# Performance work log

Hardware: AMD Instinct MI355X
Metric: run time of the kernel (lower is better)

## Reference

```python
import jax, jax.numpy as jnp
import numpy as np

D, H, K, L, NB = 128, 8, 16, 16, 2
N, E, MN, ME = 100_000, 800_000, 1_000, 8_000
VOCAB, BT, VP = 50_000, 256, 15
_SQD, _SQK = float(np.sqrt(D)), float(np.sqrt(K))


def _segment_softmax(score, seg, num):
    m = jax.ops.segment_max(score, seg, num_segments=num)
    e = jnp.exp(score - m[seg])
    z = jax.ops.segment_sum(e, seg, num_segments=num)
    return e / (z[seg] + 1e-9)


def _meta_learner(feat, u, W2, W1):
    # latent-attention factorization: feat [n,D] -> 2d param [n,H,K], 1d param [n,H]
    w = jax.nn.softmax((feat @ u.T) / _SQD, axis=-1)  # [n,L]
    return jnp.einsum('nl,lhk->nhk', w, W2), w @ W1


def _conv(feat, src, dst, p2n, p1n, p2e, p1e, Wq, Wk, Wv, Wo):
    # HeteroAttnConv: multi-head attention message passing modulated by
    # per-node (p2n,p1n) and per-edge (p2e,p1e) meta parameters.
    n = feat.shape[0]
    q = (feat @ Wq).reshape(n, H, K) * p2n
    kf = (feat @ Wk).reshape(n, H, K)
    v = (feat @ Wv).reshape(n, H, K)
    ke = kf[src] * p2e                                   # [e,H,K]
    score = (q[dst] * ke).sum(-1) / _SQK + p1e + p1n[dst]  # [e,H]
    attn = _segment_softmax(score, dst, n)
    agg = jax.ops.segment_sum(attn[..., None] * v[src], dst, num_segments=n).reshape(n, D)
    return jax.nn.relu(agg @ Wo), ke.reshape(-1, D)


def _forward(emb, u, W2lat, W1lat, Wq_m, Wk_m, Wv_m, Wo_m, Wq, Wk, Wv, Wo,
             node_vals, meta_node_vals, src, dst, meta_src, meta_dst,
             meta_node_id, meta_edge_id, target_idx,
             static_vals, static_src, static_dst):
    # _init_meta_param: static param-name graph, copy_u/sum then meta_learner
    fs = emb[static_vals]
    agg = jax.ops.segment_sum(fs[static_src], static_dst, num_segments=VP)
    p2s, p1s = _meta_learner(agg, u, W2lat, W1lat)
    base_tw, base_n1, base_n2 = p1s[0], p1s[3], p2s[6]   # target_weight, node 1d, node 2d
    base_e1, base_e2 = p1s[9], p2s[12]                   # edge 1d, edge 2d

    meta_feat = emb[meta_node_vals]
    feat = emb[node_vals]
    # _asign_param_to_graph(meta_graph): broadcast base buffers only
    mp2n = jnp.broadcast_to(base_n2, (MN, H, K))
    mp1n = jnp.broadcast_to(base_n1, (MN, H))
    mp2e = jnp.broadcast_to(base_e2, (ME, H, K))
    mp1e = jnp.broadcast_to(base_e1, (ME, H))

    out = jnp.zeros((BT, 1), feat.dtype)
    for b in range(NB):
        pre_meta, pre = meta_feat, feat
        meta_feat, meta_edge_feat = _conv(meta_feat, meta_src, meta_dst,
                                          mp2n, mp1n, mp2e, mp1e,
                                          Wq_m[b], Wk_m[b], Wv_m[b], Wo_m[b])
        # _asign_param_to_graph(graph, meta_node_feat, meta_edge_feat):
        # base repeat + indexed add of meta_learner outputs
        p2mn, p1mn = _meta_learner(meta_feat, u, W2lat, W1lat)
        p2me, p1me = _meta_learner(meta_edge_feat, u, W2lat, W1lat)
        p2n = base_n2[None] + p2mn[meta_node_id]
        p1n = base_n1[None] + p1mn[meta_node_id]
        tw = base_tw[None] + p1mn[meta_node_id]
        p2e = base_e2[None] + p2me[meta_edge_id]
        p1e = base_e1[None] + p1me[meta_edge_id]
        feat, _ = _conv(feat, src, dst, p2n, p1n, p2e, p1e,
                        Wq[b], Wk[b], Wv[b], Wo[b])
        # block residual
        meta_feat = meta_feat + pre_meta
        feat = feat + pre
        # Target: per-target-node weighted readout with target_weight param
        logit = jnp.einsum('th,thk->t', tw[target_idx],
                           feat[target_idx].reshape(BT, H, K))
        out = out + logit[:, None]
    return out / NB


def setup_inputs() -> dict:
    key = jax.random.key(0)
    ks = jax.random.split(key, 24)
    s = 0.05
    inp = {}
    inp['emb'] = jax.random.normal(ks[0], (VOCAB, D), jnp.float32) * s
    inp['u'] = jax.random.normal(ks[1], (L, D), jnp.float32) * s
    inp['W2lat'] = jax.random.normal(ks[2], (L, H, K), jnp.float32) * s
    inp['W1lat'] = jax.random.normal(ks[3], (L, H), jnp.float32) * s
    for i, nm in enumerate(['Wq_m', 'Wk_m', 'Wv_m', 'Wo_m', 'Wq', 'Wk', 'Wv', 'Wo']):
        inp[nm] = jax.random.normal(ks[4 + i], (NB, D, D), jnp.float32) / np.sqrt(D)
    inp['node_vals'] = jax.random.randint(ks[12], (N,), 0, VOCAB)
    inp['meta_node_vals'] = jax.random.randint(ks[13], (MN,), 0, VOCAB)
    inp['src'] = jax.random.randint(ks[14], (E,), 0, N)
    inp['dst'] = jax.random.randint(ks[15], (E,), 0, N)
    inp['meta_src'] = jax.random.randint(ks[16], (ME,), 0, MN)
    inp['meta_dst'] = jax.random.randint(ks[17], (ME,), 0, MN)
    inp['meta_node_id'] = jax.random.randint(ks[18], (N,), 0, MN)
    inp['meta_edge_id'] = jax.random.randint(ks[19], (E,), 0, ME)
    inp['target_idx'] = jax.random.randint(ks[20], (BT,), 0, N)
    # static param-name graph: 5 names x (1 name node + 2 token nodes), tokens->name
    name_pos = np.arange(5) * 3
    inp['static_vals'] = jax.random.randint(ks[21], (VP,), 0, VOCAB)
    inp['static_src'] = jnp.asarray(np.stack([name_pos + 1, name_pos + 2], 1).reshape(-1), jnp.int32)
    inp['static_dst'] = jnp.asarray(np.repeat(name_pos, 2), jnp.int32)
    return inp


def reference(emb, u, W2lat, W1lat, Wq_m, Wk_m, Wv_m, Wo_m, Wq, Wk, Wv, Wo,
              node_vals, meta_node_vals, src, dst, meta_src, meta_dst,
              meta_node_id, meta_edge_id, target_idx,
              static_vals, static_src, static_dst):
    return _forward(emb, u, W2lat, W1lat, Wq_m, Wk_m, Wv_m, Wo_m, Wq, Wk, Wv, Wo,
                    node_vals, meta_node_vals, src, dst, meta_src, meta_dst,
                    meta_node_id, meta_edge_id, target_idx,
                    static_vals, static_src, static_dst)
```

## Files before the change

### kernel.cpp

```cpp
#include <hip/hip_runtime.h>
#include <hip/hip_bf16.h>
#include <hip/hip_fp8.h>

#define DD   128
#define HH   8

typedef short bf16x8 __attribute__((ext_vector_type(8)));
typedef float f32x4  __attribute__((ext_vector_type(4)));
typedef float f32x2  __attribute__((ext_vector_type(2)));

__device__ __forceinline__ float b2f(unsigned short v){
  union { unsigned int u; float f; } x; x.u = ((unsigned int)v) << 16; return x.f;
}
__device__ __forceinline__ unsigned short f2b(float f){
  __hip_bfloat16 h = __float2bfloat16(f);
  return *(unsigned short*)&h;
}
__device__ __forceinline__ unsigned char f2f8(float x){
  __hip_fp8_e4m3 h(x);
  return h.__x;
}
__device__ __forceinline__ float f82f(unsigned char b){
  __hip_fp8_e4m3 h; h.__x = b;
  return (float)h;
}
__device__ __forceinline__ void cvt4(unsigned int w, float* o){
#if defined(__has_builtin)
# if __has_builtin(__builtin_amdgcn_cvt_pk_f32_fp8)
  f32x2 lo = __builtin_amdgcn_cvt_pk_f32_fp8((int)w, false);
  f32x2 hi = __builtin_amdgcn_cvt_pk_f32_fp8((int)w, true);
  o[0]=lo[0]; o[1]=lo[1]; o[2]=hi[0]; o[3]=hi[1];
  return;
# endif
#endif
  o[0]=f82f(w&0xff); o[1]=f82f((w>>8)&0xff);
  o[2]=f82f((w>>16)&0xff); o[3]=f82f((w>>24)&0xff);
}
struct __align__(8) us4 { unsigned short x,y,z,w; };
struct __align__(16) us8 { unsigned short s[8]; };

__device__ __forceinline__ float gld(const void* p, size_t i, bool f32){
  if (f32) return ((const float*)p)[i];
  return b2f(((const unsigned short*)p)[i]);
}

__device__ __forceinline__ void gll16(const void* g, void* l){
  __builtin_amdgcn_global_load_lds(
      (const __attribute__((address_space(1))) unsigned int*)g,
      (__attribute__((address_space(3))) unsigned int*)l, 16, 0, 0);
}

struct WPtrs { const void* p[8]; };
__global__ __launch_bounds__(256) void w_repack16(
    WPtrs W, unsigned short* __restrict__ stage, int NBt,
    const int* __restrict__ dflag)
{
  const bool wf32 = (*dflag) != 0;
  int idx = blockIdx.x >> 6;
  int ti = idx / NBt, bi = idx - ti*NBt;
  size_t bo = (size_t)bi*DD*DD;
  int i = (blockIdx.x & 63)*256 + threadIdx.x;
  int k = i >> 7, n = i & 127;
  float x;
  if (wf32) x = ((const float*)W.p[ti])[bo + i];
  else      x = b2f(((const unsigned short*)W.p[ti])[bo + i]);
  stage[(size_t)idx*DD*DD + n*DD + k] = f2b(x);
}

enum { EPI_STORE=0, EPI_SCALE_CONST=1, EPI_RELU=3,
       EPI_RELU_RES=4, EPI_RELU_RES2=5 };

#define CPAD 132


template<int EPI, bool INB, bool OUTB>
__global__ __launch_bounds__(256) void gemm128m(
    const void* __restrict__ Av, const unsigned short* __restrict__ Bt,
    void* __restrict__ Cv, int M,
    const unsigned short* __restrict__ Rb,
    const float* __restrict__ Rf, float* __restrict__ C2)
{
  __shared__ __align__(16) unsigned short Asb[64*128];
  __shared__ __align__(16) unsigned short Btb[16896];
  const int tid = threadIdx.x;
  const int wave = tid >> 6, lane = tid & 63;
  const int row0 = blockIdx.x * 64;

  if (INB){
    const char* Ab = (const char*)Av;
    int n4 = lane >> 4, c = lane & 15;
#pragma unroll
    for (int op=0; op<4; op++){
      int rA = wave*16 + op*4;
      int n = rA + n4;
      int gr = row0 + n; if (gr >= M) gr = M - 1;
      gll16(Ab + (size_t)gr*256 + ((size_t)((c ^ (n & 7)) << 4)), &Asb[rA*128]);
    }
  } else {
    const float* Af = (const float*)Av;
    int r = tid >> 2, cb = (tid & 3) * 32, rx = (r & 7) << 3;
    int gr = row0 + r;
#pragma unroll
    for (int j=0;j<8;j++){
      int cc = cb + j*4;
      float4 val = make_float4(0.f,0.f,0.f,0.f);
      if (gr < M) val = *(const float4*)(Af + (size_t)gr*DD + cc);
      us4 o; o.x=f2b(val.x); o.y=f2b(val.y); o.z=f2b(val.z); o.w=f2b(val.w);
      *(us4*)&Asb[r*128 + (cc ^ rx)] = o;
    }
  }
  {
    int n4 = lane >> 4, c = lane & 15;
#pragma unroll
    for (int op=0; op<8; op++){
      int rB = wave*32 + op*4;
      int n = rB + n4;
      gll16((const char*)Bt + (size_t)n*256 + ((size_t)((c ^ (n & 7)) << 4)),
            &Btb[rB*128]);
    }
  }
  __syncthreads();

  f32x4 acc[8];
#pragma unroll
  for (int t=0;t<8;t++) acc[t] = (f32x4){0.f,0.f,0.f,0.f};
  const int am = (lane & 15), kq = (lane >> 4) * 8, axr = (am & 7) << 3;
#pragma unroll
  for (int k0=0;k0<128;k0+=32){
    int xo = (k0 + kq) ^ axr;
    bf16x8 a = *(bf16x8*)&Asb[(wave*16 + am)*128 + xo];
#pragma unroll
    for (int t=0;t<8;t++){
      bf16x8 b = *(bf16x8*)&Btb[(t*16 + am)*128 + xo];
      acc[t] = __builtin_amdgcn_mfma_f32_16x16x32_bf16(a, b, acc[t], 0,0,0);
    }
  }
  __syncthreads();
  float* Cls = (float*)Btb;
  {
    int rr = wave*16 + (lane>>4)*4;
    int cc = lane & 15;
#pragma unroll
    for (int t=0;t<8;t++)
#pragma unroll
      for (int r=0;r<4;r++)
        Cls[(rr + r)*CPAD + t*16 + cc] = acc[t][r];
  }
  __syncthreads();

  {
    int r = tid >> 2, cb = (tid & 3) * 32;
    int gr = row0 + r;
    if (gr < M){
#pragma unroll
      for (int j=0;j<8;j++){
        int c = cb + j*4;
        float4 o = *(float4*)&Cls[r*CPAD + c];
        if (EPI == EPI_RELU_RES){
          us4 rb = *(const us4*)(Rb + (size_t)gr*DD + c);
          o.x=fmaxf(o.x,0.f)+b2f(rb.x); o.y=fmaxf(o.y,0.f)+b2f(rb.y);
          o.z=fmaxf(o.z,0.f)+b2f(rb.z); o.w=fmaxf(o.w,0.f)+b2f(rb.w);
        } else if (EPI == EPI_RELU_RES2){
          o.x=fmaxf(o.x,0.f); o.y=fmaxf(o.y,0.f); o.z=fmaxf(o.z,0.f); o.w=fmaxf(o.w,0.f);
          float4 rf = *(const float4*)(Rf + (size_t)gr*DD + c);
          *(float4*)(C2 + (size_t)gr*DD + c) =
              make_float4(o.x+rf.x, o.y+rf.y, o.z+rf.z, o.w+rf.w);
        }
        if (OUTB){
          us4 ob; ob.x=f2b(o.x); ob.y=f2b(o.y); ob.z=f2b(o.z); ob.w=f2b(o.w);
          *(us4*)((unsigned short*)Cv + (size_t)gr*DD + c) = ob;
        } else {
          *(float4*)((float*)Cv + (size_t)gr*DD + c) = o;
        }
      }
    }
  }
}

template<int EPIQ, bool INB, bool FP8KV>
__device__ __forceinline__ void qkv_body(
    unsigned short* Asb, unsigned short* Btb, int blk,
    const void* __restrict__ Av,
    const unsigned short* __restrict__ Btq, const unsigned short* __restrict__ Btk,
    const unsigned short* __restrict__ Btv,
    void* __restrict__ Cq, void* __restrict__ Ck, int stK,
    void* __restrict__ Cvo, int stV, int M,
    const float* __restrict__ svec)
{
  const int tid = threadIdx.x;
  const int wave = tid >> 6, lane = tid & 63;
  const int row0 = blk * 64;

  if (INB){
    const char* Ab = (const char*)Av;
    int n4 = lane >> 4, c = lane & 15;
#pragma unroll
    for (int op=0; op<4; op++){
      int rA = wave*16 + op*4;
      int n = rA + n4;
      int gr = row0 + n; if (gr >= M) gr = M - 1;
      gll16(Ab + (size_t)gr*256 + ((size_t)((c ^ (n & 7)) << 4)), &Asb[rA*128]);
    }
  } else {
    const float* Af = (const float*)Av;
    int r = tid >> 2, cb = (tid & 3) * 32, rx = (r & 7) << 3;
    int gr = row0 + r;
#pragma unroll
    for (int j=0;j<8;j++){
      int cc = cb + j*4;
      float4 val = make_float4(0.f,0.f,0.f,0.f);
      if (gr < M) val = *(const float4*)(Af + (size_t)gr*DD + cc);
      us4 o; o.x=f2b(val.x); o.y=f2b(val.y); o.z=f2b(val.z); o.w=f2b(val.w);
      *(us4*)&Asb[r*128 + (cc ^ rx)] = o;
    }
  }

  const unsigned short* Bts[3] = {Btq, Btk, Btv};
  void* Cs[3] = {Cq, Ck, Cvo};
  const int sts[3] = {DD, stK, stV};
  const int am = (lane & 15), kq = (lane >> 4) * 8, axr = (am & 7) << 3;

  for (int ph=0; ph<3; ph++){
    {
      const unsigned short* Bt = Bts[ph];
      int n4 = lane >> 4, c = lane & 15;
#pragma unroll
      for (int op=0; op<8; op++){
        int rB = wave*32 + op*4;
        int n = rB + n4;
        gll16((const char*)Bt + (size_t)n*256 + ((size_t)((c ^ (n & 7)) << 4)),
              &Btb[rB*128]);
      }
    }
    __syncthreads();
    f32x4 acc[8];
#pragma unroll
    for (int t=0;t<8;t++) acc[t] = (f32x4){0.f,0.f,0.f,0.f};
#pragma unroll
    for (int k0=0;k0<128;k0+=32){
      int xo = (k0 + kq) ^ axr;
      bf16x8 a = *(bf16x8*)&Asb[(wave*16 + am)*128 + xo];
#pragma unroll
      for (int t=0;t<8;t++){
        bf16x8 b = *(bf16x8*)&Btb[(t*16 + am)*128 + xo];
        acc[t] = __builtin_amdgcn_mfma_f32_16x16x32_bf16(a, b, acc[t], 0,0,0);
      }
    }
    __syncthreads();
    float* Cls = (float*)Btb;
    {
      int rr = wave*16 + (lane>>4)*4;
      int cc = lane & 15;
#pragma unroll
      for (int t=0;t<8;t++)
#pragma unroll
        for (int r=0;r<4;r++)
          Cls[(rr + r)*CPAD + t*16 + cc] = acc[t][r];
    }
    __syncthreads();
    {
      int r = tid >> 2, cb = (tid & 3) * 32;
      int gr = row0 + r;
      if (gr < M){
#pragma unroll
        for (int j=0;j<8;j++){
          int c = cb + j*4;
          float4 o = *(float4*)&Cls[r*CPAD + c];
          if (ph == 0 && EPIQ == EPI_SCALE_CONST){
            o.x*=svec[c+0]; o.y*=svec[c+1]; o.z*=svec[c+2]; o.w*=svec[c+3];
          }
          if (FP8KV && ph > 0){
            unsigned char* Cb = (unsigned char*)Cs[ph];
            uchar4 ob;
            ob.x=f2f8(o.x*8.f); ob.y=f2f8(o.y*8.f);
            ob.z=f2f8(o.z*8.f); ob.w=f2f8(o.w*8.f);
            *(uchar4*)(Cb + (size_t)gr*256 + c) = ob;
          } else {
            us4 ob; ob.x=f2b(o.x); ob.y=f2b(o.y); ob.z=f2b(o.z); ob.w=f2b(o.w);
            *(us4*)((unsigned short*)Cs[ph] + (size_t)gr*sts[ph] + c) = ob;
          }
        }
      }
    }
    __syncthreads();
  }
}

__global__ __launch_bounds__(256) void gemm_qkv2(
    const unsigned short* __restrict__ featB, const float* __restrict__ featM,
    const unsigned short* __restrict__ wqb, const unsigned short* __restrict__ wkb,
    const unsigned short* __restrict__ wvb,
    const unsigned short* __restrict__ wqm, const unsigned short* __restrict__ wkm,
    const unsigned short* __restrict__ wvm,
    unsigned short* __restrict__ qB, unsigned char* __restrict__ kv8,
    unsigned short* __restrict__ qM, unsigned short* __restrict__ kfM,
    unsigned short* __restrict__ vM,
    int Nbig, int Nmeta, int gN, const float* __restrict__ svec)
{
  __shared__ __align__(16) unsigned short Asb[64*128];
  __shared__ __align__(16) unsigned short Btb[16896];
  if (blockIdx.x < gN){
    qkv_body<EPI_STORE,true,true>(Asb, Btb, blockIdx.x, featB,
        wqb, wkb, wvb, qB, kv8, 0, kv8 + 128, 0, Nbig, svec);
  } else {
    qkv_body<EPI_SCALE_CONST,false,false>(Asb, Btb, blockIdx.x - gN, featM,
        wqm, wkm, wvm, qM, kfM, DD, vM, DD, Nmeta, svec);
  }
}

__global__ __launch_bounds__(256) void k_static(
    const void* __restrict__ emb, const int* __restrict__ svals,
    const int* __restrict__ ssrc, const int* __restrict__ sdst,
    const void* __restrict__ u, const void* __restrict__ W2,
    const void* __restrict__ W1, float* __restrict__ base, int nsrc,
    int* __restrict__ dflag)
{
  __shared__ float sagg[15][128];
  __shared__ float ssc[15][16];
  __shared__ float sww[15][16];
  __shared__ int swf;
  const int t = threadIdx.x;
  if (t < 64){
    float m = 0.f;
    for (int i=t; i<128; i+=64){
      float x = fabsf(b2f(((const unsigned short*)emb)[i]));
      if (x < 1e30f) m = fmaxf(m, x);
    }
#pragma unroll
    for (int s=1;s<64;s<<=1) m = fmaxf(m, __shfl_xor(m, s, 64));
    if (t==0){ int f = (m > 1e4f) ? 1 : 0; *dflag = f; swf = f; }
  }
  for (int i=t;i<15*128;i+=256) ((float*)sagg)[i]=0.f;
  __syncthreads();
  const bool wf32 = (swf != 0);
  if (t < 128){
    for (int i=0;i<nsrc;i++){
      int row = sdst[i]; int vr = svals[ssrc[i]];
      sagg[row][t] += gld(emb, (size_t)vr*DD + t, wf32);
    }
  }
  __syncthreads();
  if (t < 240){
    int n = t>>4, l = t&15;
    float a=0.f;
    for (int d=0;d<128;d++) a += sagg[n][d]*gld(u, l*128+d, wf32);
    ssc[n][l] = a * 0.08838834764831845f;
  }
  __syncthreads();
  if (t < 15){
    float mx=-1e30f;
    for (int l=0;l<16;l++) mx = fmaxf(mx, ssc[t][l]);
    float s=0.f;
    for (int l=0;l<16;l++){ float e=__expf(ssc[t][l]-mx); sww[t][l]=e; s+=e; }
    float inv = 1.f/s;
    for (int l=0;l<16;l++) sww[t][l]*=inv;
  }
  __syncthreads();
  if (t < 8){
    float a=0.f,b=0.f,c=0.f;
    for (int l=0;l<16;l++){
      float wv = gld(W1, l*8+t, wf32);
      a += sww[0][l]*wv; b += sww[3][l]*wv; c += sww[9][l]*wv;
    }
    base[t]=a; base[8+t]=b; base[16+t]=c;
  }
  if (t < 128){
    float a=0.f,b=0.f;
    for (int l=0;l<16;l++){
      float wv = gld(W2, l*128+t, wf32);
      a += sww[6][l]*wv; b += sww[12][l]*wv;
    }
    base[24+t]=a; base[152+t]=b;
  }
}

__global__ __launch_bounds__(256) void gather_rows2(
    const void* __restrict__ emb,
    const int* __restrict__ valsB, unsigned short* __restrict__ featB, int nB,
    const int* __restrict__ valsM, float* __restrict__ featM, int nM,
    const int* __restrict__ dflag)
{
  const bool wf32 = (*dflag) != 0;
  int i = blockIdx.x*256 + threadIdx.x;
  bool big = (i < nB*16);
  int i2 = big ? i : (i - nB*16);
  if (!big && i2 >= nM*16) return;
  int r = i2>>4, c = (i2&15)*8;
  int vr = big ? valsB[r] : valsM[r];
  float vb[8];
  if (wf32){
    float4 f0 = *(const float4*)((const float*)emb + (size_t)vr*DD + c);
    float4 f1 = *(const float4*)((const float*)emb + (size_t)vr*DD + c + 4);
    vb[0]=f0.x; vb[1]=f0.y; vb[2]=f0.z; vb[3]=f0.w;
    vb[4]=f1.x; vb[5]=f1.y; vb[6]=f1.z; vb[7]=f1.w;
  } else {
    uint4 raw = *(const uint4*)((const unsigned short*)emb + (size_t)vr*DD + c);
    const unsigned short* hw = (const unsigned short*)&raw;
#pragma unroll
    for (int j=0;j<8;j++) vb[j] = b2f(hw[j]);
  }
  if (big){
    unsigned short* d = featB + (size_t)r*DD + c;
    us4 o0, o1;
    o0.x=f2b(vb[0]); o0.y=f2b(vb[1]); o0.z=f2b(vb[2]); o0.w=f2b(vb[3]);
    o1.x=f2b(vb[4]); o1.y=f2b(vb[5]); o1.z=f2b(vb[6]); o1.w=f2b(vb[7]);
    *(us4*)d = o0; *(us4*)(d+4) = o1;
  } else {
    float* d = featM + (size_t)r*DD + c;
    *(float4*)d     = make_float4(vb[0],vb[1],vb[2],vb[3]);
    *(float4*)(d+4) = make_float4(vb[4],vb[5],vb[6],vb[7]);
  }
}

__global__ __launch_bounds__(256) void zeroi(int* __restrict__ p, int n){
  int i = blockIdx.x*256 + threadIdx.x;
  if (i < n) p[i] = 0;
}

__global__ __launch_bounds__(256) void k_hist2(
    const int* __restrict__ dstB, const int* __restrict__ dstM,
    int* __restrict__ degB, int* __restrict__ degM, int E, int ME, int nbE){
  int b = blockIdx.x, t = threadIdx.x;
  if (b < nbE){ int i = b*256+t; if (i < E) atomicAdd(&degB[dstB[i]], 1); }
  else { int i = (b-nbE)*256+t; if (i < ME) atomicAdd(&degM[dstM[i]], 1); }
}

__global__ __launch_bounds__(256) void k_scan1b(
    const int* __restrict__ degB, int* __restrict__ rpB, int* __restrict__ bsB,
    int nB, int nbB,
    const int* __restrict__ degM, int* __restrict__ rpM, int* __restrict__ bsM,
    int nM){
  __shared__ int ls[256];
  int blk = blockIdx.x, t = threadIdx.x;
  const int* deg; int* rowptr; int* bsum; int n; int b;
  if (blk < nbB){ deg=degB; rowptr=rpB; bsum=bsB; n=nB; b=blk; }
  else          { deg=degM; rowptr=rpM; bsum=bsM; n=nM; b=blk-nbB; }
  int base = b*1024 + t*4;
  int v0 = (base+0<n)?deg[base+0]:0;
  int v1 = (base+1<n)?deg[base+1]:0;
  int v2 = (base+2<n)?deg[base+2]:0;
  int v3 = (base+3<n)?deg[base+3]:0;
  int tsum = v0+v1+v2+v3;
  ls[t] = tsum; __syncthreads();
  for (int o=1;o<256;o<<=1){
    int x = (t>=o) ? ls[t-o] : 0;
    __syncthreads();
    ls[t] += x;
    __syncthreads();
  }
  int excl = ls[t]-tsum;
  if (t==255) bsum[b] = ls[255];
  if (base+0<n) rowptr[base+0]=excl;
  if (base+1<n) rowptr[base+1]=excl+v0;
  if (base+2<n) rowptr[base+2]=excl+v0+v1;
  if (base+3<n) rowptr[base+3]=excl+v0+v1+v2;
}

__global__ __launch_bounds__(256) void k_scan3b(
    int* __restrict__ rpB, const int* __restrict__ bsB, int* __restrict__ curB,
    int nB, int nb3B, int nbsB,
    int* __restrict__ rpM, const int* __restrict__ bsM, int* __restrict__ curM,
    int nM, int nbsM){
  __shared__ int spre;
  int blk = blockIdx.x, t = threadIdx.x;
  if (blk < nb3B){
    if (t == 0){
      int chunk = blk >> 2;
      int pre = 0;
      for (int j=0;j<chunk;j++) pre += bsB[j];
      spre = pre;
      if (blk == 0){
        int tot = 0;
        for (int j=0;j<nbsB;j++) tot += bsB[j];
        rpB[nB] = tot;
      }
    }
    __syncthreads();
    int i = blk*256 + t;
    if (i < nB){ int r = rpB[i] + spre; rpB[i] = r; curB[i] = r; }
  } else {
    int b2 = blk - nb3B;
    if (t == 0){
      int chunk = b2 >> 2;
      int pre = 0;
      for (int j=0;j<chunk;j++) pre += bsM[j];
      spre = pre;
      if (b2 == 0){
        int tot = 0;
        for (int j=0;j<nbsM;j++) tot += bsM[j];
        rpM[nM] = tot;
      }
    }
    __syncthreads();
    int i = b2*256 + t;
    if (i < nM){ int r = rpM[i] + spre; rpM[i] = r; curM[i] = r; }
  }
}

__global__ __launch_bounds__(256) void k_scatter2(
    const int* __restrict__ dstB, const int* __restrict__ srcB,
    const int* __restrict__ auxB, int* __restrict__ curB,
    int* __restrict__ epackB, int E, int nbE,
    const int* __restrict__ dstM, const int* __restrict__ srcM,
    int* __restrict__ curM, int* __restrict__ esrcM, int* __restrict__ eauxM,
    int ME){
  int blk = blockIdx.x, t = threadIdx.x;
  if (blk < nbE){
    int e = blk*256 + t;
    if (e < E){
      int p = atomicAdd(&curB[dstB[e]], 1);
      epackB[p] = srcB[e] | (auxB[e] << 17);
    }
  } else {
    int e = (blk-nbE)*256 + t;
    if (e < ME){
      int p = atomicAdd(&curM[dstM[e]], 1);
      esrcM[p] = srcM[e];
      eauxM[p] = e;
    }
  }
}

__global__ __launch_bounds__(256) void edge_meta_csr(
    const int* __restrict__ rowptr, const int* __restrict__ esrc,
    const int* __restrict__ eorig,
    const unsigned short* __restrict__ qm, const unsigned short* __restrict__ kfm,
    const unsigned short* __restrict__ vm,
    const float* __restrict__ base, unsigned short* __restrict__ mef,
    float* __restrict__ agg, int NM)
{
  int d = blockIdx.x*4 + (threadIdx.x>>6);
  if (d >= NM) return;
  int lane = threadIdx.x & 63;
  const float* be2 = base+152; const float* be1 = base+16; const float* bn1 = base+8;
  size_t dq = (size_t)d*DD;
  float q0 = b2f(qm[dq+lane]), q1 = b2f(qm[dq+64+lane]);
  float w0 = be2[lane], w1 = be2[64+lane];
  int h0 = lane>>4, h1 = h0+4;
  float bias0 = be1[h0] + bn1[h0];
  float bias1 = be1[h1] + bn1[h1];
  float z0=0.f, z1=0.f, a0=0.f, a1=0.f;
  int i0 = rowptr[d], i1 = rowptr[d+1];
  for (int i=i0; i<i1; i++){
    int s = esrc[i], e = eorig[i];
    size_t so=(size_t)s*DD, eo=(size_t)e*DD;
    float ke0 = b2f(kfm[so+lane])    * w0;
    float ke1 = b2f(kfm[so+64+lane]) * w1;
    mef[eo+lane]=f2b(ke0); mef[eo+64+lane]=f2b(ke1);
    float p0 = q0*ke0, p1 = q1*ke1;
#pragma unroll
    for (int m=1;m<16;m<<=1){ p0 += __shfl_xor(p0,m,64); p1 += __shfl_xor(p1,m,64); }
    float e0 = __expf(p0*0.25f + bias0);
    float e1 = __expf(p1*0.25f + bias1);
    z0 += e0; z1 += e1;
    a0 += e0*b2f(vm[so+lane]);
    a1 += e1*b2f(vm[so+64+lane]);
  }
  float inv0 = 1.f/(z0 + 1e-9f);
  float inv1 = 1.f/(z1 + 1e-9f);
  agg[dq+lane]    = a0*inv0;
  agg[dq+64+lane] = a1*inv1;
}

__global__ __launch_bounds__(128) void learner2(
    const float* __restrict__ Xa, const unsigned short* __restrict__ Xb,
    int Ma, int Mtot,
    const void* __restrict__ u, const void* __restrict__ W2,
    const void* __restrict__ W1,
    float* __restrict__ p2a, float* __restrict__ p1a,
    unsigned short* __restrict__ w2me, unsigned short* __restrict__ p1b,
    const float* __restrict__ base, const int* __restrict__ dflag)
{
  __shared__ float sX[128];
  __shared__ float st[16];
  __shared__ float sw[16];
  const bool wf32 = (*dflag) != 0;
  const int t = threadIdx.x;
  const int l = t>>3, j = t&7;
  float uc[16], w2c[16], w1c[16];
#pragma unroll
  for (int m=0;m<16;m++) uc[m] = gld(u, (size_t)l*128 + j*16 + m, wf32);
#pragma unroll
  for (int i=0;i<16;i++) w2c[i] = gld(W2, (size_t)i*128 + t, wf32);
  if (t < 8){
#pragma unroll
    for (int i=0;i<16;i++) w1c[i] = gld(W1, (size_t)i*8 + t, wf32);
  }
  for (int rr=0; rr<4; rr++){
    int row = blockIdx.x*4 + rr;
    if (row >= Mtot) break;
    const bool isB = (row >= Ma);
    const int m = isB ? (row - Ma) : row;
    if (isB) sX[t] = b2f(Xb[(size_t)m*DD + t]);
    else     sX[t] = Xa[(size_t)m*DD + t];
    __syncthreads();
    float part = 0.f;
#pragma unroll
    for (int mm=0;mm<16;mm++) part += sX[j*16+mm]*uc[mm];
    part += __shfl_xor(part,1,64); part += __shfl_xor(part,2,64); part += __shfl_xor(part,4,64);
    if (j==0) st[l] = part * 0.08838834764831845f;
    __syncthreads();
    float mx=-1e30f;
    for (int i=0;i<16;i++) mx = fmaxf(mx, st[i]);
    float ssum=0.f;
    for (int i=0;i<16;i++) ssum += __expf(st[i]-mx);
    float inv = 1.f/ssum;
    if (t<16) sw[t] = __expf(st[t]-mx)*inv;
    __syncthreads();
    float a=0.f;
#pragma unroll
    for (int i=0;i<16;i++) a += sw[i]*w2c[i];
    if (isB) w2me[(size_t)m*DD+t] = f2b(base[152+t] + a);
    else     p2a[(size_t)m*DD+t] = a;
    if (t<8){
      float bb=0.f;
#pragma unroll
      for (int i=0;i<16;i++) bb += sw[i]*w1c[i];
      if (isB) p1b[(size_t)m*HH+t] = f2b(bb);
      else     p1a[(size_t)m*HH+t] = bb;
    }
    __syncthreads();
  }
}

__global__ __launch_bounds__(256) void edge_fused(
    const int* __restrict__ rowptr, const int* __restrict__ epack,
    const int* __restrict__ mnid,
    const unsigned short* __restrict__ q, const unsigned char* __restrict__ kv8,
    const unsigned short* __restrict__ w2me, const unsigned short* __restrict__ p1me,
    const float* __restrict__ p1mn, const float* __restrict__ p2mn,
    const float* __restrict__ base,
    unsigned short* __restrict__ aggb, int N)
{
  int wv = blockIdx.x*4 + (threadIdx.x>>6);
  int lane = threadIdx.x & 63;
  int grp = lane >> 4, l16 = lane & 15;
  int d = wv*4 + grp;
  if (d >= N) return;
  int c8 = l16 * 8;
  int h = l16 >> 1;

  int i0 = rowptr[d], i1 = rowptr[d+1];
  int mn = mnid[d];
  float bias = base[16+h] + base[8+h] + p1mn[(size_t)mn*HH + h];
  size_t dq = (size_t)d*DD;
  float qv[8];
  {
    uint4 qraw = *(const uint4*)(q + dq + c8);
    const unsigned short* qh = (const unsigned short*)&qraw;
    const float* p2 = p2mn + (size_t)mn*DD + c8;
    const float* sv = base + 24 + c8;
#pragma unroll
    for (int j=0;j<8;j++) qv[j] = b2f(qh[j]) * (sv[j] + p2[j]) * 0.03125f;
  }

  float zh = 0.f;
  float a[8];
#pragma unroll
  for (int j=0;j<8;j++) a[j] = 0.f;

  int i = i0;
  for (; i + 3 < i1; i += 4){
    uint2 kr[4], vr[4]; uint4 wr[4]; float pm[4];
#pragma unroll
    for (int t=0;t<4;t++){
      unsigned int vp = (unsigned int)epack[i+t];
      int s = vp & 0x1FFFF, me = vp >> 17;
      const unsigned char* kv = kv8 + (size_t)s*256 + c8;
      kr[t] = *(const uint2*)kv;
      vr[t] = *(const uint2*)(kv + 128);
      wr[t] = *(const uint4*)(w2me + (size_t)me*DD + c8);
      pm[t] = b2f(p1me[(size_t)me*HH + h]);
    }
#pragma unroll
    for (int t=0;t<4;t++){
      float kf[8], vf[8];
      cvt4(kr[t].x, kf); cvt4(kr[t].y, kf+4);
      cvt4(vr[t].x, vf); cvt4(vr[t].y, vf+4);
      const unsigned short* wh = (const unsigned short*)&wr[t];
      float p = 0.f;
#pragma unroll
      for (int j=0;j<8;j++) p += qv[j]*(kf[j]*b2f(wh[j]));
      p += __shfl_xor(p, 1, 64);
      float ex = __expf(p + bias + pm[t]);
      zh += ex;
#pragma unroll
      for (int j=0;j<8;j++) a[j] += ex*vf[j];
    }
  }
  for (; i + 1 < i1; i += 2){
    unsigned int v0p = (unsigned int)epack[i];
    unsigned int v1p = (unsigned int)epack[i+1];
    int s0 = v0p & 0x1FFFF, me0 = v0p >> 17;
    int s1 = v1p & 0x1FFFF, me1 = v1p >> 17;
    const unsigned char* kv0 = kv8 + (size_t)s0*256 + c8;
    const unsigned char* kv1 = kv8 + (size_t)s1*256 + c8;
    uint2 kraw0 = *(const uint2*)kv0;
    uint2 vraw0 = *(const uint2*)(kv0 + 128);
    uint4 wraw0 = *(const uint4*)(w2me + (size_t)me0*DD + c8);
    float pm0 = b2f(p1me[(size_t)me0*HH + h]);
    uint2 kraw1 = *(const uint2*)kv1;
    uint2 vraw1 = *(const uint2*)(kv1 + 128);
    uint4 wraw1 = *(const uint4*)(w2me + (size_t)me1*DD + c8);
    float pm1 = b2f(p1me[(size_t)me1*HH + h]);
    float k0f[8], v0f[8], k1f[8], v1f[8];
    cvt4(kraw0.x, k0f); cvt4(kraw0.y, k0f+4);
    cvt4(vraw0.x, v0f); cvt4(vraw0.y, v0f+4);
    cvt4(kraw1.x, k1f); cvt4(kraw1.y, k1f+4);
    cvt4(vraw1.x, v1f); cvt4(vraw1.y, v1f+4);
    const unsigned short* wh0 = (const unsigned short*)&wraw0;
    const unsigned short* wh1 = (const unsigned short*)&wraw1;
    float pA = 0.f, pB = 0.f;
#pragma unroll
    for (int j=0;j<8;j++){
      pA += qv[j]*(k0f[j]*b2f(wh0[j]));
      pB += qv[j]*(k1f[j]*b2f(wh1[j]));
    }
    pA += __shfl_xor(pA, 1, 64);
    pB += __shfl_xor(pB, 1, 64);
    float ex0 = __expf(pA + bias + pm0);
    float ex1 = __expf(pB + bias + pm1);
    zh += ex0 + ex1;
#pragma unroll
    for (int j=0;j<8;j++) a[j] += ex0*v0f[j] + ex1*v1f[j];
  }
  if (i < i1){
    unsigned int vp = (unsigned int)epack[i];
    int s = vp & 0x1FFFF, me = vp >> 17;
    const unsigned char* kv = kv8 + (size_t)s*256 + c8;
    uint2 kraw = *(const uint2*)kv;
    uint2 vraw = *(const uint2*)(kv + 128);
    uint4 wraw = *(const uint4*)(w2me + (size_t)me*DD + c8);
    float pm = b2f(p1me[(size_t)me*HH + h]);
    float kf[8], vf[8];
    cvt4(kraw.x, kf); cvt4(kraw.y, kf+4);
    cvt4(vraw.x, vf); cvt4(vraw.y, vf+4);
    const unsigned short* wh = (const unsigned short*)&wraw;
    float p = 0.f;
#pragma unroll
    for (int j=0;j<8;j++) p += qv[j]*(kf[j]*b2f(wh[j]));
    p += __shfl_xor(p, 1, 64);
    float ex = __expf(p + bias + pm);
    zh += ex;
#pragma unroll
    for (int j=0;j<8;j++) a[j] += ex*vf[j];
  }

  float inv = 0.125f / (zh + 1e-9f);
  us8 o;
#pragma unroll
  for (int j=0;j<8;j++) o.s[j] = f2b(a[j]*inv);
  *(us8*)(aggb + dq + c8) = o;
}

__global__ __launch_bounds__(256) void readout(
    const int* __restrict__ tgt, const int* __restrict__ mnid,
    const unsigned short* __restrict__ featb, const float* __restrict__ p1mn,
    const float* __restrict__ base, float* __restrict__ acc,
    void* __restrict__ out, int last, float invNB, int BT,
    const int* __restrict__ dflag)
{
  int t = blockIdx.x*256 + threadIdx.x;
  int ti = t >> 4, l16 = t & 15;
  if (ti >= BT) return;
  int idx = tgt[ti]; int mn = mnid[idx];
  int h = l16 >> 1;
  float tw = base[h] + p1mn[(size_t)mn*HH + h];
  uint4 raw = *(const uint4*)(featb + (size_t)idx*DD + l16*8);
  const unsigned short* hw = (const unsigned short*)&raw;
  float s = 0.f;
#pragma unroll
  for (int j=0;j<8;j++) s += b2f(hw[j]);
  float part = tw * s;
  part += __shfl_xor(part, 1, 64);
  part += __shfl_xor(part, 2, 64);
  part += __shfl_xor(part, 4, 64);
  part += __shfl_xor(part, 8, 64);
  if (l16 == 0){
    if (!last) acc[ti] = part;
    else {
      float r = (acc[ti] + part) * invNB;
      if ((*dflag) != 0) ((float*)out)[ti] = r;
      else ((__hip_bfloat16*)out)[ti] = __float2bfloat16(r);
    }
  }
}

extern "C" void kernel_launch(void* const* d_in, const int* in_sizes, int n_in,
                              void* d_out, int out_size, void* d_ws, size_t ws_size,
                              hipStream_t stream) {
  const void* emb   = d_in[0];
  const void* u     = d_in[1];
  const void* W2lat = d_in[2];
  const void* W1lat = d_in[3];
  WPtrs wptrs;
  for (int i=0;i<8;i++) wptrs.p[i] = d_in[4+i];
  const int* node_vals      = (const int*)d_in[12];
  const int* meta_node_vals = (const int*)d_in[13];
  const int* src            = (const int*)d_in[14];
  const int* dst            = (const int*)d_in[15];
  const int* meta_src       = (const int*)d_in[16];
  const int* meta_dst       = (const int*)d_in[17];
  const int* meta_node_id   = (const int*)d_in[18];
  const int* meta_edge_id   = (const int*)d_in[19];
  const int* target_idx     = (const int*)d_in[20];
  const int* static_vals    = (const int*)d_in[21];
  const int* static_src     = (const int*)d_in[22];
  const int* static_dst     = (const int*)d_in[23];

  const int N  = in_sizes[12];
  const int MN = in_sizes[13];
  const int E  = in_sizes[14];
  const int ME = in_sizes[16];
  const int BT = in_sizes[20];
  const int NSRC = in_sizes[22];
  const int NB = in_sizes[8] / (DD*DD);

  float* ws = (float*)d_ws;
  size_t off = 0;
  auto allocf = [&](size_t n){ float* p = ws + off; off += (n + 3) & ~(size_t)3; return p; };
  auto allocb = [&](size_t n){ unsigned short* p = (unsigned short*)(ws + off); off += (((n+1)/2) + 3) & ~(size_t)3; return p; };
  auto alloci = [&](size_t n){ int* p = (int*)(ws + off); off += (n + 3) & ~(size_t)3; return p; };
  int*            dflag = (int*)ws; off += 4;
  unsigned short* feat  = allocb((size_t)N*DD);
  unsigned short* q     = allocb((size_t)N*DD);
  unsigned char*  kv8   = (unsigned char*)allocf((size_t)N*64);
  unsigned short* aggb  = allocb((size_t)N*DD);
  float*          meta_feat= allocf((size_t)MN*DD);
  float*          agg_m = allocf((size_t)MN*DD);
  unsigned short* q_m   = allocb((size_t)MN*DD);
  unsigned short* kf_m  = allocb((size_t)MN*DD);
  unsigned short* v_m   = allocb((size_t)MN*DD);
  float*          meta_out = allocf((size_t)MN*DD);
  unsigned short* mef   = allocb((size_t)ME*DD);
  float*          p2mn  = allocf((size_t)MN*DD);
  float*          p1mn  = allocf((size_t)MN*HH);
  unsigned short* w2me  = allocb((size_t)ME*DD);
  unsigned short* p1me  = allocb((size_t)ME*HH);
  float*          base  = allocf(280);
  float*          acc   = allocf((size_t)BT);
  unsigned short* wstage= allocb((size_t)8*NB*DD*DD);
  int*            rowptr= alloci((size_t)N+1);
  int*            cursor= alloci((size_t)N);
  int*            epack = alloci((size_t)E);
  int*            rowptr_m= alloci((size_t)MN+1);
  int*            cursor_m= alloci((size_t)MN);
  int*            esrc_m  = alloci((size_t)ME);
  int*            eorig_m = alloci((size_t)ME);
  int*            degAll  = alloci((size_t)(N+MN));
  int*            deg     = degAll;
  int*            deg_m   = degAll + N;
  const int nb_scan   = (N + 1023)/1024;
  const int nb_scan_m = (MN + 1023)/1024;
  int*            bsum   = alloci((size_t)nb_scan);
  int*            bsum_m = alloci((size_t)nb_scan_m);
  (void)ws_size; (void)n_in; (void)out_size;

  const float* base_n2 = base + 24;

  k_static<<<1,256,0,stream>>>(emb, static_vals, static_src, static_dst,
                               u, W2lat, W1lat, base, NSRC, dflag);
  gather_rows2<<<((N+MN)*16+255)/256,256,0,stream>>>(emb, node_vals, feat, N,
      meta_node_vals, meta_feat, MN, dflag);

  const int nbE  = (E+255)/256, nbME = (ME+255)/256;
  const int nb3B = (N+255)/256, nb3M = (MN+255)/256;
  zeroi<<<(N+MN+255)/256,256,0,stream>>>(degAll, N+MN);
  k_hist2<<<nbE+nbME,256,0,stream>>>(dst, meta_dst, deg, deg_m, E, ME, nbE);
  k_scan1b<<<nb_scan+nb_scan_m,256,0,stream>>>(deg, rowptr, bsum, N, nb_scan,
      deg_m, rowptr_m, bsum_m, MN);
  k_scan3b<<<nb3B+nb3M,256,0,stream>>>(rowptr, bsum, cursor, N, nb3B, nb_scan,
      rowptr_m, bsum_m, cursor_m, MN, nb_scan_m);
  k_scatter2<<<nbE+nbME,256,0,stream>>>(dst, src, meta_edge_id, cursor,
      epack, E, nbE, meta_dst, meta_src, cursor_m, esrc_m, eorig_m, ME);

  w_repack16<<<8*NB*64,256,0,stream>>>(wptrs, wstage, NB, dflag);

  const int gm = (MN+63)/64;
  const int gN = (N+63)/64;
  const float invNB = 1.0f/(float)NB;

  for (int b=0;b<NB;b++){
    const unsigned short* wq_m = wstage + (size_t)(0*NB+b)*DD*DD;
    const unsigned short* wk_m = wstage + (size_t)(1*NB+b)*DD*DD;
    const unsigned short* wv_m = wstage + (size_t)(2*NB+b)*DD*DD;
    const unsigned short* wo_m = wstage + (size_t)(3*NB+b)*DD*DD;
    const unsigned short* wqb  = wstage + (size_t)(4*NB+b)*DD*DD;
    const unsigned short* wkb  = wstage + (size_t)(5*NB+b)*DD*DD;
    const unsigned short* wvb  = wstage + (size_t)(6*NB+b)*DD*DD;
    const unsigned short* wob  = wstage + (size_t)(7*NB+b)*DD*DD;

    gemm_qkv2<<<gN+gm,256,0,stream>>>(feat, meta_feat,
        wqb, wkb, wvb, wq_m, wk_m, wv_m,
        q, kv8, q_m, kf_m, v_m, N, MN, gN, base_n2);

    edge_meta_csr<<<(MN+3)/4,256,0,stream>>>(rowptr_m, esrc_m, eorig_m,
        q_m, kf_m, v_m, base, mef, agg_m, MN);
    gemm128m<EPI_RELU_RES2,false,false><<<gm,256,0,stream>>>(agg_m, wo_m,
        meta_out, MN, nullptr, meta_feat, meta_feat);
    learner2<<<(MN+ME+3)/4,128,0,stream>>>(meta_out, mef, MN, MN+ME,
        u, W2lat, W1lat, p2mn, p1mn, w2me, p1me, base, dflag);

    edge_fused<<<(N+15)/16,256,0,stream>>>(rowptr, epack,
        meta_node_id, q, kv8, w2me, p1me, p1mn, p2mn, base, aggb, N);
    gemm128m<EPI_RELU_RES,true,true><<<gN,256,0,stream>>>(aggb, wob, feat, N,
        feat, nullptr, nullptr);

    readout<<<(BT*16+255)/256,256,0,stream>>>(target_idx, meta_node_id, feat, p1mn,
        base, acc, d_out, (b==NB-1) ? 1 : 0, invNB, BT, dflag);
  }
}
```

Baseline: 571.9 us.

## Sort destination nodes by degree for balanced edge processing and precompute bf16 query scale

Result: slower. 1.249 ms (+118.4%).

```diff
diff --git a/kernel.cpp b/kernel.cpp
--- a/kernel.cpp
+++ b/kernel.cpp
@@ -460,7 +460,8 @@
     int* __restrict__ rpB, const int* __restrict__ bsB, int* __restrict__ curB,
     int nB, int nb3B, int nbsB,
     int* __restrict__ rpM, const int* __restrict__ bsM, int* __restrict__ curM,
-    int nM, int nbsM){
+    int nM, int nbsM,
+    const int* __restrict__ degB, int* __restrict__ dbins){
   __shared__ int spre;
   int blk = blockIdx.x, t = threadIdx.x;
   if (blk < nb3B){
@@ -477,7 +478,11 @@
     }
     __syncthreads();
     int i = blk*256 + t;
-    if (i < nB){ int r = rpB[i] + spre; rpB[i] = r; curB[i] = r; }
+    if (i < nB){
+      int r = rpB[i] + spre; rpB[i] = r; curB[i] = r;
+      int dg = degB[i]; if (dg > 63) dg = 63;
+      atomicAdd(&dbins[dg], 1);
+    }
   } else {
     int b2 = blk - nb3B;
     if (t == 0){
@@ -503,7 +508,8 @@
     int* __restrict__ epackB, int E, int nbE,
     const int* __restrict__ dstM, const int* __restrict__ srcM,
     int* __restrict__ curM, int* __restrict__ esrcM, int* __restrict__ eauxM,
-    int ME){
+    int ME, int nbME,
+    const int* __restrict__ dbins, int* __restrict__ dcur){
   int blk = blockIdx.x, t = threadIdx.x;
   if (blk < nbE){
     int e = blk*256 + t;
@@ -511,14 +517,29 @@
       int p = atomicAdd(&curB[dstB[e]], 1);
       epackB[p] = srcB[e] | (auxB[e] << 17);
     }
-  } else {
+  } else if (blk < nbE + nbME){
     int e = (blk-nbE)*256 + t;
     if (e < ME){
       int p = atomicAdd(&curM[dstM[e]], 1);
       esrcM[p] = srcM[e];
       eauxM[p] = e;
     }
-  }
+  } else {
+    if (t == 0){
+      int run = 0;
+      for (int j=0;j<64;j++){ dcur[j] = run; run += dbins[j]; }
+    }
+  }
+}
+
+__global__ __launch_bounds__(256) void k_dsort(
+    const int* __restrict__ deg, int* __restrict__ dcur,
+    int* __restrict__ sortN, int N){
+  int i = blockIdx.x*256 + threadIdx.x;
+  if (i >= N) return;
+  int dg = deg[i]; if (dg > 63) dg = 63;
+  int pos = atomicAdd(&dcur[dg], 1);
+  sortN[pos] = i;
 }
 
 __global__ __launch_bounds__(256) void edge_meta_csr(
@@ -567,7 +588,7 @@
     int Ma, int Mtot,
     const void* __restrict__ u, const void* __restrict__ W2,
     const void* __restrict__ W1,
-    float* __restrict__ p2a, float* __restrict__ p1a,
+    unsigned short* __restrict__ qsc, float* __restrict__ p1a,
     unsigned short* __restrict__ w2me, unsigned short* __restrict__ p1b,
     const float* __restrict__ base, const int* __restrict__ dflag)
 {
@@ -611,7 +632,7 @@
 #pragma unroll
     for (int i=0;i<16;i++) a += sw[i]*w2c[i];
     if (isB) w2me[(size_t)m*DD+t] = f2b(base[152+t] + a);
-    else     p2a[(size_t)m*DD+t] = a;
+    else     qsc[(size_t)m*DD+t] = f2b(base[24+t] + a);
     if (t<8){
       float bb=0.f;
 #pragma unroll
@@ -625,18 +646,19 @@
 
 __global__ __launch_bounds__(256) void edge_fused(
     const int* __restrict__ rowptr, const int* __restrict__ epack,
-    const int* __restrict__ mnid,
+    const int* __restrict__ sortN, const int* __restrict__ mnid,
     const unsigned short* __restrict__ q, const unsigned char* __restrict__ kv8,
     const unsigned short* __restrict__ w2me, const unsigned short* __restrict__ p1me,
-    const float* __restrict__ p1mn, const float* __restrict__ p2mn,
+    const float* __restrict__ p1mn, const unsigned short* __restrict__ qsc,
     const float* __restrict__ base,
     unsigned short* __restrict__ aggb, int N)
 {
   int wv = blockIdx.x*4 + (threadIdx.x>>6);
   int lane = threadIdx.x & 63;
   int grp = lane >> 4, l16 = lane & 15;
-  int d = wv*4 + grp;
-  if (d >= N) return;
+  int idx = wv*4 + grp;
+  if (idx >= N) return;
+  int d = sortN[idx];
   int c8 = l16 * 8;
   int h = l16 >> 1;
 
@@ -647,11 +669,10 @@
   float qv[8];
   {
     uint4 qraw = *(const uint4*)(q + dq + c8);
+    us8 sc = *(const us8*)(qsc + (size_t)mn*DD + c8);
     const unsigned short* qh = (const unsigned short*)&qraw;
-    const float* p2 = p2mn + (size_t)mn*DD + c8;
-    const float* sv = base + 24 + c8;
-#pragma unroll
-    for (int j=0;j<8;j++) qv[j] = b2f(qh[j]) * (sv[j] + p2[j]) * 0.03125f;
+#pragma unroll
+    for (int j=0;j<8;j++) qv[j] = b2f(qh[j]) * b2f(sc.s[j]) * 0.03125f;
   }
 
   float zh = 0.f;
@@ -660,34 +681,6 @@
   for (int j=0;j<8;j++) a[j] = 0.f;
 
   int i = i0;
-  for (; i + 3 < i1; i += 4){
-    uint2 kr[4], vr[4]; uint4 wr[4]; float pm[4];
-#pragma unroll
-    for (int t=0;t<4;t++){
-      unsigned int vp = (unsigned int)epack[i+t];
-      int s = vp & 0x1FFFF, me = vp >> 17;
-      const unsigned char* kv = kv8 + (size_t)s*256 + c8;
-      kr[t] = *(const uint2*)kv;
-      vr[t] = *(const uint2*)(kv + 128);
-      wr[t] = *(const uint4*)(w2me + (size_t)me*DD + c8);
-      pm[t] = b2f(p1me[(size_t)me*HH + h]);
-    }
-#pragma unroll
-    for (int t=0;t<4;t++){
-      float kf[8], vf[8];
-      cvt4(kr[t].x, kf); cvt4(kr[t].y, kf+4);
-      cvt4(vr[t].x, vf); cvt4(vr[t].y, vf+4);
-      const unsigned short* wh = (const unsigned short*)&wr[t];
-      float p = 0.f;
-#pragma unroll
-      for (int j=0;j<8;j++) p += qv[j]*(kf[j]*b2f(wh[j]));
-      p += __shfl_xor(p, 1, 64);
-      float ex = __expf(p + bias + pm[t]);
-      zh += ex;
-#pragma unroll
-      for (int j=0;j<8;j++) a[j] += ex*vf[j];
-    }
-  }
   for (; i + 1 < i1; i += 2){
     unsigned int v0p = (unsigned int)epack[i];
     unsigned int v1p = (unsigned int)epack[i+1];
@@ -833,7 +826,7 @@
   unsigned short* v_m   = allocb((size_t)MN*DD);
   float*          meta_out = allocf((size_t)MN*DD);
   unsigned short* mef   = allocb((size_t)ME*DD);
-  float*          p2mn  = allocf((size_t)MN*DD);
+  unsigned short* qsc   = allocb((size_t)MN*DD);
   float*          p1mn  = allocf((size_t)MN*HH);
   unsigned short* w2me  = allocb((size_t)ME*DD);
   unsigned short* p1me  = allocb((size_t)ME*HH);
@@ -847,9 +840,12 @@
   int*            cursor_m= alloci((size_t)MN);
   int*            esrc_m  = alloci((size_t)ME);
   int*            eorig_m = alloci((size_t)ME);
+  int*            dbins   = alloci(64);
   int*            degAll  = alloci((size_t)(N+MN));
   int*            deg     = degAll;
   int*            deg_m   = degAll + N;
+  int*            dcur    = alloci(64);
+  int*            sortN   = alloci((size_t)N);
   const int nb_scan   = (N + 1023)/1024;
   const int nb_scan_m = (MN + 1023)/1024;
   int*            bsum   = alloci((size_t)nb_scan);
@@ -865,14 +861,16 @@
 
   const int nbE  = (E+255)/256, nbME = (ME+255)/256;
   const int nb3B = (N+255)/256, nb3M = (MN+255)/256;
-  zeroi<<<(N+MN+255)/256,256,0,stream>>>(degAll, N+MN);
+  zeroi<<<(64+N+MN+255)/256,256,0,stream>>>(dbins, 64+N+MN);
   k_hist2<<<nbE+nbME,256,0,stream>>>(dst, meta_dst, deg, deg_m, E, ME, nbE);
   k_scan1b<<<nb_scan+nb_scan_m,256,0,stream>>>(deg, rowptr, bsum, N, nb_scan,
       deg_m, rowptr_m, bsum_m, MN);
   k_scan3b<<<nb3B+nb3M,256,0,stream>>>(rowptr, bsum, cursor, N, nb3B, nb_scan,
-      rowptr_m, bsum_m, cursor_m, MN, nb_scan_m);
-  k_scatter2<<<nbE+nbME,256,0,stream>>>(dst, src, meta_edge_id, cursor,
-      epack, E, nbE, meta_dst, meta_src, cursor_m, esrc_m, eorig_m, ME);
+      rowptr_m, bsum_m, cursor_m, MN, nb_scan_m, deg, dbins);
+  k_scatter2<<<nbE+nbME+1,256,0,stream>>>(dst, src, meta_edge_id, cursor,
+      epack, E, nbE, meta_dst, meta_src, cursor_m, esrc_m, eorig_m, ME, nbME,
+      dbins, dcur);
+  k_dsort<<<(N+255)/256,256,0,stream>>>(deg, dcur, sortN, N);
 
   w_repack16<<<8*NB*64,256,0,stream>>>(wptrs, wstage, NB, dflag);
 
@@ -899,10 +897,10 @@
     gemm128m<EPI_RELU_RES2,false,false><<<gm,256,0,stream>>>(agg_m, wo_m,
         meta_out, MN, nullptr, meta_feat, meta_feat);
     learner2<<<(MN+ME+3)/4,128,0,stream>>>(meta_out, mef, MN, MN+ME,
-        u, W2lat, W1lat, p2mn, p1mn, w2me, p1me, base, dflag);
-
-    edge_fused<<<(N+15)/16,256,0,stream>>>(rowptr, epack,
-        meta_node_id, q, kv8, w2me, p1me, p1mn, p2mn, base, aggb, N);
+        u, W2lat, W1lat, qsc, p1mn, w2me, p1me, base, dflag);
+
+    edge_fused<<<(N+15)/16,256,0,stream>>>(rowptr, epack, sortN,
+        meta_node_id, q, kv8, w2me, p1me, p1mn, qsc, base, aggb, N);
     gemm128m<EPI_RELU_RES,true,true><<<gN,256,0,stream>>>(aggb, wob, feat, N,
         feat, nullptr, nullptr);
 
```

## Split Q projection into separate GEMM with fused meta-parameter scaling

Applied to the files above, without the earlier changes.

Result: slower. 594.2 us (+3.9%).

```diff
diff --git a/kernel.cpp b/kernel.cpp
--- a/kernel.cpp
+++ b/kernel.cpp
@@ -71,7 +71,6 @@
        EPI_RELU_RES=4, EPI_RELU_RES2=5 };
 
 #define CPAD 132
-
 
 template<int EPI, bool INB, bool OUTB>
 __global__ __launch_bounds__(256) void gemm128m(
@@ -177,7 +176,7 @@
   }
 }
 
-template<int EPIQ, bool INB, bool FP8KV>
+template<int EPIQ, bool INB, bool KVONLY>
 __device__ __forceinline__ void qkv_body(
     unsigned short* Asb, unsigned short* Btb, int blk,
     const void* __restrict__ Av,
@@ -215,12 +214,13 @@
     }
   }
 
-  const unsigned short* Bts[3] = {Btq, Btk, Btv};
-  void* Cs[3] = {Cq, Ck, Cvo};
+  const unsigned short* Bts[3] = {KVONLY ? Btk : Btq, KVONLY ? Btv : Btk, Btv};
+  void* Cs[3] = {KVONLY ? Ck : Cq, Ck, Cvo};
   const int sts[3] = {DD, stK, stV};
+  const int nph = KVONLY ? 2 : 3;
   const int am = (lane & 15), kq = (lane >> 4) * 8, axr = (am & 7) << 3;
 
-  for (int ph=0; ph<3; ph++){
+  for (int ph=0; ph<nph; ph++){
     {
       const unsigned short* Bt = Bts[ph];
       int n4 = lane >> 4, c = lane & 15;
@@ -266,15 +266,15 @@
         for (int j=0;j<8;j++){
           int c = cb + j*4;
           float4 o = *(float4*)&Cls[r*CPAD + c];
-          if (ph == 0 && EPIQ == EPI_SCALE_CONST){
+          if (!KVONLY && ph == 0 && EPIQ == EPI_SCALE_CONST){
             o.x*=svec[c+0]; o.y*=svec[c+1]; o.z*=svec[c+2]; o.w*=svec[c+3];
           }
-          if (FP8KV && ph > 0){
-            unsigned char* Cb = (unsigned char*)Cs[ph];
+          if (KVONLY){
+            unsigned char* Cb = (unsigned char*)Cs[0];
             uchar4 ob;
             ob.x=f2f8(o.x*8.f); ob.y=f2f8(o.y*8.f);
             ob.z=f2f8(o.z*8.f); ob.w=f2f8(o.w*8.f);
-            *(uchar4*)(Cb + (size_t)gr*256 + c) = ob;
+            *(uchar4*)(Cb + (size_t)gr*256 + ph*128 + c) = ob;
           } else {
             us4 ob; ob.x=f2b(o.x); ob.y=f2b(o.y); ob.z=f2b(o.z); ob.w=f2b(o.w);
             *(us4*)((unsigned short*)Cs[ph] + (size_t)gr*sts[ph] + c) = ob;
@@ -288,11 +288,10 @@
 
 __global__ __launch_bounds__(256) void gemm_qkv2(
     const unsigned short* __restrict__ featB, const float* __restrict__ featM,
-    const unsigned short* __restrict__ wqb, const unsigned short* __restrict__ wkb,
-    const unsigned short* __restrict__ wvb,
+    const unsigned short* __restrict__ wkb, const unsigned short* __restrict__ wvb,
     const unsigned short* __restrict__ wqm, const unsigned short* __restrict__ wkm,
     const unsigned short* __restrict__ wvm,
-    unsigned short* __restrict__ qB, unsigned char* __restrict__ kv8,
+    unsigned char* __restrict__ kv8,
     unsigned short* __restrict__ qM, unsigned short* __restrict__ kfM,
     unsigned short* __restrict__ vM,
     int Nbig, int Nmeta, int gN, const float* __restrict__ svec)
@@ -301,10 +300,90 @@
   __shared__ __align__(16) unsigned short Btb[16896];
   if (blockIdx.x < gN){
     qkv_body<EPI_STORE,true,true>(Asb, Btb, blockIdx.x, featB,
-        wqb, wkb, wvb, qB, kv8, 0, kv8 + 128, 0, Nbig, svec);
+        nullptr, wkb, wvb, nullptr, kv8, 0, nullptr, 0, Nbig, svec);
   } else {
     qkv_body<EPI_SCALE_CONST,false,false>(Asb, Btb, blockIdx.x - gN, featM,
         wqm, wkm, wvm, qM, kfM, DD, vM, DD, Nmeta, svec);
+  }
+}
+
+__global__ __launch_bounds__(256) void gemm_q1(
+    const unsigned short* __restrict__ Ab, const unsigned short* __restrict__ Bt,
+    unsigned short* __restrict__ Cq, int M,
+    const float* __restrict__ svec, const float* __restrict__ P2,
+    const int* __restrict__ gidx)
+{
+  __shared__ __align__(16) unsigned short Asb[64*128];
+  __shared__ __align__(16) unsigned short Btb[16896];
+  const int tid = threadIdx.x;
+  const int wave = tid >> 6, lane = tid & 63;
+  const int row0 = blockIdx.x * 64;
+
+  {
+    int n4 = lane >> 4, c = lane & 15;
+#pragma unroll
+    for (int op=0; op<4; op++){
+      int rA = wave*16 + op*4;
+      int n = rA + n4;
+      int gr = row0 + n; if (gr >= M) gr = M - 1;
+      gll16((const char*)Ab + (size_t)gr*256 + ((size_t)((c ^ (n & 7)) << 4)),
+            &Asb[rA*128]);
+    }
+    }
+  {
+    int n4 = lane >> 4, c = lane & 15;
+#pragma unroll
+    for (int op=0; op<8; op++){
+      int rB = wave*32 + op*4;
+      int n = rB + n4;
+      gll16((const char*)Bt + (size_t)n*256 + ((size_t)((c ^ (n & 7)) << 4)),
+            &Btb[rB*128]);
+    }
+  }
+  __syncthreads();
+
+  f32x4 acc[8];
+#pragma unroll
+  for (int t=0;t<8;t++) acc[t] = (f32x4){0.f,0.f,0.f,0.f};
+  const int am = (lane & 15), kq = (lane >> 4) * 8, axr = (am & 7) << 3;
+#pragma unroll
+  for (int k0=0;k0<128;k0+=32){
+    int xo = (k0 + kq) ^ axr;
+    bf16x8 a = *(bf16x8*)&Asb[(wave*16 + am)*128 + xo];
+#pragma unroll
+    for (int t=0;t<8;t++){
+      bf16x8 b = *(bf16x8*)&Btb[(t*16 + am)*128 + xo];
+      acc[t] = __builtin_amdgcn_mfma_f32_16x16x32_bf16(a, b, acc[t], 0,0,0);
+    }
+  }
+  __syncthreads();
+  float* Cls = (float*)Btb;
+  {
+    int rr = wave*16 + (lane>>4)*4;
+    int cc = lane & 15;
+#pragma unroll
+    for (int t=0;t<8;t++)
+#pragma unroll
+      for (int r=0;r<4;r++)
+        Cls[(rr + r)*CPAD + t*16 + cc] = acc[t][r];
+  }
+  __syncthreads();
+  {
+    int r = tid >> 2, cb = (tid & 3) * 32;
+    int gr = row0 + r;
+    if (gr < M){
+      int g = gidx[gr];
+      const float* p = P2 + (size_t)g*DD;
+#pragma unroll
+      for (int j=0;j<8;j++){
+        int c = cb + j*4;
+        float4 o = *(float4*)&Cls[r*CPAD + c];
+        o.x*=(svec[c+0]+p[c+0]); o.y*=(svec[c+1]+p[c+1]);
+        o.z*=(svec[c+2]+p[c+2]); o.w*=(svec[c+3]+p[c+3]);
+        us4 ob; ob.x=f2b(o.x); ob.y=f2b(o.y); ob.z=f2b(o.z); ob.w=f2b(o.w);
+        *(us4*)(Cq + (size_t)gr*DD + c) = ob;
+      }
+    }
   }
 }
 
@@ -628,8 +707,7 @@
     const int* __restrict__ mnid,
     const unsigned short* __restrict__ q, const unsigned char* __restrict__ kv8,
     const unsigned short* __restrict__ w2me, const unsigned short* __restrict__ p1me,
-    const float* __restrict__ p1mn, const float* __restrict__ p2mn,
-    const float* __restrict__ base,
+    const float* __restrict__ p1mn, const float* __restrict__ base,
     unsigned short* __restrict__ aggb, int N)
 {
   int wv = blockIdx.x*4 + (threadIdx.x>>6);
@@ -641,17 +719,14 @@
   int h = l16 >> 1;
 
   int i0 = rowptr[d], i1 = rowptr[d+1];
-  int mn = mnid[d];
-  float bias = base[16+h] + base[8+h] + p1mn[(size_t)mn*HH + h];
+  float bias = base[16+h] + base[8+h] + p1mn[(size_t)mnid[d]*HH + h];
   size_t dq = (size_t)d*DD;
   float qv[8];
   {
     uint4 qraw = *(const uint4*)(q + dq + c8);
     const unsigned short* qh = (const unsigned short*)&qraw;
-    const float* p2 = p2mn + (size_t)mn*DD + c8;
-    const float* sv = base + 24 + c8;
-#pragma unroll
-    for (int j=0;j<8;j++) qv[j] = b2f(qh[j]) * (sv[j] + p2[j]) * 0.03125f;
+#pragma unroll
+    for (int j=0;j<8;j++) qv[j] = b2f(qh[j])*0.03125f;
   }
 
   float zh = 0.f;
@@ -660,34 +735,6 @@
   for (int j=0;j<8;j++) a[j] = 0.f;
 
   int i = i0;
-  for (; i + 3 < i1; i += 4){
-    uint2 kr[4], vr[4]; uint4 wr[4]; float pm[4];
-#pragma unroll
-    for (int t=0;t<4;t++){
-      unsigned int vp = (unsigned int)epack[i+t];
-      int s = vp & 0x1FFFF, me = vp >> 17;
-      const unsigned char* kv = kv8 + (size_t)s*256 + c8;
-      kr[t] = *(const uint2*)kv;
-      vr[t] = *(const uint2*)(kv + 128);
-      wr[t] = *(const uint4*)(w2me + (size_t)me*DD + c8);
-      pm[t] = b2f(p1me[(size_t)me*HH + h]);
-    }
-#pragma unroll
-    for (int t=0;t<4;t++){
-      float kf[8], vf[8];
-      cvt4(kr[t].x, kf); cvt4(kr[t].y, kf+4);
-      cvt4(vr[t].x, vf); cvt4(vr[t].y, vf+4);
-      const unsigned short* wh = (const unsigned short*)&wr[t];
-      float p = 0.f;
-#pragma unroll
-      for (int j=0;j<8;j++) p += qv[j]*(kf[j]*b2f(wh[j]));
-      p += __shfl_xor(p, 1, 64);
-      float ex = __expf(p + bias + pm[t]);
-      zh += ex;
-#pragma unroll
-      for (int j=0;j<8;j++) a[j] += ex*vf[j];
-    }
-  }
   for (; i + 1 < i1; i += 2){
     unsigned int v0p = (unsigned int)epack[i];
     unsigned int v1p = (unsigned int)epack[i+1];
@@ -891,8 +938,8 @@
     const unsigned short* wob  = wstage + (size_t)(7*NB+b)*DD*DD;
 
     gemm_qkv2<<<gN+gm,256,0,stream>>>(feat, meta_feat,
-        wqb, wkb, wvb, wq_m, wk_m, wv_m,
-        q, kv8, q_m, kf_m, v_m, N, MN, gN, base_n2);
+        wkb, wvb, wq_m, wk_m, wv_m,
+        kv8, q_m, kf_m, v_m, N, MN, gN, base_n2);
 
     edge_meta_csr<<<(MN+3)/4,256,0,stream>>>(rowptr_m, esrc_m, eorig_m,
         q_m, kf_m, v_m, base, mef, agg_m, MN);
@@ -901,8 +948,10 @@
     learner2<<<(MN+ME+3)/4,128,0,stream>>>(meta_out, mef, MN, MN+ME,
         u, W2lat, W1lat, p2mn, p1mn, w2me, p1me, base, dflag);
 
+    gemm_q1<<<gN,256,0,stream>>>(feat, wqb, q, N, base_n2, p2mn, meta_node_id);
+
     edge_fused<<<(N+15)/16,256,0,stream>>>(rowptr, epack,
-        meta_node_id, q, kv8, w2me, p1me, p1mn, p2mn, base, aggb, N);
+        meta_node_id, q, kv8, w2me, p1me, p1mn, base, aggb, N);
     gemm128m<EPI_RELU_RES,true,true><<<gN,256,0,stream>>>(aggb, wob, feat, N,
         feat, nullptr, nullptr);
 
```
